# Kernel tuning notes

Hardware: AMD Instinct MI355X
Metric: run time of the kernel (lower is better)

Reference implementation:

```python
import jax, jax.numpy as jnp
import numpy as np

ALPHA = 0.01
EPSB = ALPHA / (1.0 - 2.0 * ALPHA)  # boundary_eps
BIG = 1e9  # stands in for +inf; all real boundary distances are << box diameter


def setup_inputs() -> dict:
    key = jax.random.key(0)
    ks = jax.random.split(key, 8)
    B, D, K = 32768, 16, 1024
    return {
        "x": jax.random.normal(ks[0], (B, D), jnp.float32),
        "logp": jnp.zeros((B, 1), jnp.float32),
        "an1_w": 0.1 * jax.random.normal(ks[1], (D,), jnp.float32),
        "an1_b": 0.1 * jax.random.normal(ks[2], (D,), jnp.float32),
        "an2_w": 0.1 * jax.random.normal(ks[3], (D,), jnp.float32),
        "an2_b": 0.1 * jax.random.normal(ks[4], (D,), jnp.float32),
        "shift_coeff": jax.random.normal(ks[5], (D,), jnp.float32),
        "anchor_raw": jax.random.normal(ks[6], (1, K, D), jnp.float32),  # vorproj._anchor_pts
        "box_min": -4.0 * jnp.ones((D,), jnp.float32),
        "box_max": 4.0 * jnp.ones((D,), jnp.float32),
        "mixture_logits": jnp.zeros((K,), jnp.float32),
    }


def reference(x, logp, an1_w, an1_b, an2_w, an2_b, shift_coeff,
              anchor_raw, box_min, box_max, mixture_logits):
    B, D = x.shape
    # --- actnorm1: y = (x + b) * exp(w); logdet = sum(w) ---
    x = (x + an1_b) * jnp.exp(an1_w)
    logp = logp - jnp.sum(an1_w)
    # --- logit_transform.inverse: y = (sigmoid(x) - alpha) / (1 - 2*alpha) ---
    ld = jnp.sum(jax.nn.log_sigmoid(x) + jax.nn.log_sigmoid(-x), axis=1, keepdims=True) \
         - D * jnp.log(1.0 - 2.0 * ALPHA)
    x = (jax.nn.sigmoid(x) - ALPHA) / (1.0 - 2.0 * ALPHA)
    logp = logp - ld
    # --- (-eps, 1+eps) -> (0, 1) ---
    span = 1.0 + 2.0 * EPSB
    x = (x + EPSB) / span
    logp = logp + D * jnp.log(span)
    # --- scale into box constraints ---
    scale = box_max - box_min  # (D,)
    x = x * scale + box_min
    logp = logp - jnp.sum(jnp.log(scale))
    # --- anchor points: R -> (-1,1) -> (0,1) -> box ---
    a = anchor_raw[0]                       # (K, D)
    a = a / (1.0 + jnp.abs(a))
    a = (a + 1.0) * 0.5 * scale + box_min   # (K, D)
    K = a.shape[0]
    # --- find_nearest: argmin_k ||x - a_k||^2 (drop const ||x||^2) ---
    a_sq = jnp.sum(a * a, axis=1)                    # (K,)
    d2 = a_sq[None, :] - 2.0 * (x @ a.T)             # (B, K)
    k = jnp.argmin(d2, axis=1)                       # (B,)
    mask = jax.nn.one_hot(k, K, dtype=bool).reshape(B, 1, K)
    x_k = a[k]                                       # (B, D) gathered anchor
    # --- shift toward anchor: x + c*(x_k - x); logdet = sum log(1-c) ---
    c = jax.nn.sigmoid(shift_coeff) * 0.98 + 0.01
    x = x + c * (x_k - x)
    logp = logp - jnp.sum(jnp.log1p(-c))
    # --- map_outside_cell: radial map of Voronoi cell (within box) onto R^D ---
    dx = x - x_k
    r = jnp.sqrt(jnp.sum(dx * dx, axis=1))           # (B,)
    u = dx / jnp.maximum(r, 1e-12)[:, None]          # (B, D) unit direction
    # half-plane boundary distance t_j = (||a_j - a_k||^2 / 2) / (u . (a_j - a_k))
    proj = u @ a.T - jnp.sum(u * x_k, axis=1, keepdims=True)              # (B, K)
    halfdist = 0.5 * (a_sq[None, :] + a_sq[k][:, None] - 2.0 * (x_k @ a.T))  # (B, K)
    self_mask = jnp.arange(K)[None, :] == k[:, None]
    valid = jnp.logical_and(jnp.logical_not(self_mask), proj > 1e-12)
    t_half = jnp.where(valid, halfdist / jnp.where(valid, proj, 1.0), BIG)
    # box-face distances along u
    up = u > 1e-12
    un = u < -1e-12
    t_box = jnp.where(up, (box_max[None, :] - x_k) / jnp.where(up, u, 1.0),
            jnp.where(un, (box_min[None, :] - x_k) / jnp.where(un, u, 1.0), BIG))
    t = jnp.minimum(jnp.min(t_half, axis=1), jnp.min(t_box, axis=1))      # (B,)
    ratio = r / t                                     # in [0, 0.99] after shift
    s = 1.0 / (1.0 - ratio)
    x = x_k + dx * s[:, None]
    # logdet = (D+1) * log(t / (t - r)) = -(D+1) * log1p(-ratio)
    logp = logp + (D + 1.0) * jnp.log1p(-ratio)[:, None]
    # --- subtract cell center ---
    x = x - x_k
    # --- actnorm2 ---
    x = (x + an2_b) * jnp.exp(an2_w)
    logp = logp - jnp.sum(an2_w)
    # --- mixture component log-prob ---
    logprobs = jax.nn.log_softmax(mixture_logits)
    logp = logp - logprobs[k][:, None]
    return x, logp, mask
```

## Files before the change

### kernel.cpp

```cpp
#include <hip/hip_runtime.h>
#include <math.h>

#define DD 16
#define KK 1024

typedef float f2 __attribute__((ext_vector_type(2)));

#define WS_A    0
#define WS_ASQ  16384
#define WS_OMC  17408
#define WS_B2   17424
#define WS_E2   17440
#define WS_MN   17456
#define WS_MX   17472
#define WS_SCL  17488
#define WS_DIM  17504
#define WS_E1   17520
#define WS_BASE 17536
#define WS_TOTD 17537
#define WS_NEED_BYTES (WS_TOTD * 8)

__device__ __forceinline__ double xformD(double rv, double mn, double scl) {
  double t = rv / (1.0 + fabs(rv));
  return (t + 1.0) * 0.5 * scl + mn;
}
__device__ __forceinline__ float xformF(float v, float mn, float mx) {
  return (v / (1.f + fabsf(v)) + 1.f) * 0.5f * (mx - mn) + mn;
}

__global__ __launch_bounds__(256) void vor_pre(
    const float* __restrict__ an1_w, const float* __restrict__ an2_w,
    const float* __restrict__ an2_b, const float* __restrict__ shift_c,
    const float* __restrict__ anchor_raw,
    const float* __restrict__ box_min, const float* __restrict__ box_max,
    const float* __restrict__ mlogits, double* __restrict__ ws)
{
  __shared__ double redD[16];
  const int tid = threadIdx.x;
  const int blk = blockIdx.x;

  if (blk == 0 && tid < DD) {
    double w1 = (double)an1_w[tid], w2 = (double)an2_w[tid];
    double sgc = 1.0 / (1.0 + exp(-(double)shift_c[tid]));
    double c = sgc * 0.98 + 0.01;
    double mn = (double)box_min[tid], mx = (double)box_max[tid];
    ws[WS_OMC + tid] = 1.0 - c;
    ws[WS_B2  + tid] = (double)an2_b[tid];
    ws[WS_E2  + tid] = exp(w2);
    ws[WS_MN  + tid] = mn;
    ws[WS_MX  + tid] = mx;
    ws[WS_SCL + tid] = mx - mn;
    ws[WS_E1  + tid] = exp(w1);
    ws[WS_DIM + tid] = -w1 - log(mx - mn) - log1p(-c) - w2;
  }
  const int j0 = blk * 64;
  for (int e = tid; e < 64 * DD; e += 256) {
    int j = j0 + (e >> 4), d = e & 15;
    double mn = (double)box_min[d];
    double scl = (double)box_max[d] - mn;
    ws[WS_A + (size_t)j * DD + d] = xformD((double)anchor_raw[j * DD + d], mn, scl);
  }
  __syncthreads();
  for (int j = j0 + tid; j < j0 + 64; j += 256) {
    double s = 0.0;
    #pragma unroll
    for (int d = 0; d < DD; ++d) { double a = ws[WS_A + (size_t)j * DD + d]; s = fma(a, a, s); }
    ws[WS_ASQ + j] = s;
  }
  if (blk != 0) return;
  float lm = -3.4e38f;
  for (int i = tid; i < KK; i += 256) lm = fmaxf(lm, mlogits[i]);
  #pragma unroll
  for (int o = 32; o > 0; o >>= 1) lm = fmaxf(lm, __shfl_xor(lm, o));
  if ((tid & 63) == 0) redD[tid >> 6] = (double)lm;
  __syncthreads();
  float gmax = (float)fmax(fmax(redD[0], redD[1]), fmax(redD[2], redD[3]));
  double lsum = 0.0;
  for (int i = tid; i < KK; i += 256) lsum += exp((double)mlogits[i] - (double)gmax);
  #pragma unroll
  for (int o = 32; o > 0; o >>= 1) lsum += __shfl_xor(lsum, o);
  if ((tid & 63) == 0) redD[4 + (tid >> 6)] = lsum;
  __syncthreads();
  if (tid == 0) {
    double lse = (double)gmax + log(redD[4] + redD[5] + redD[6] + redD[7]);
    double b = (double)DD * (log(0.98) + log(1.0 + 2.0 * (0.01 / 0.98)));
    #pragma unroll
    for (int d = 0; d < DD; ++d) b += ws[WS_DIM + d];
    ws[WS_BASE] = b + lse;
  }
}

#define NT2 1024
#define RPB2 128
#define SL2 8
#define JSL2 (KK / SL2)

__global__ __launch_bounds__(NT2, 4) void vor6(
    const float* __restrict__ x_in, const float* __restrict__ logp_in,
    const float* __restrict__ an1_b,
    const float* __restrict__ mlogits, const double* __restrict__ ws,
    float* __restrict__ out, int Brows)
{
  __shared__ __align__(16) float sAp[KK][DD];
  __shared__ float  sAsqH[KK];
  __shared__ double sX4D[DD][RPB2];
  __shared__ float  sLT[DD][RPB2];
  __shared__ double sD2[16][64];
  __shared__ int    sJJ[16][64];
  __shared__ float  sRat[16][64];
  __shared__ float  sOmcF[DD], sB2F[DD], sE2F[DD], sMnF[DD], sMxF[DD];

  const int tid  = threadIdx.x;
  const int w    = tid >> 6;
  const int lane = tid & 63;
  const int rg   = w >> 3;
  const int sl   = w & 7;
  const int rrow = rg * 64 + lane;
  const int row  = blockIdx.x * RPB2 + rrow;
  const size_t coreEnd = (size_t)Brows * (DD + 1);

  if (tid < DD) {
    sOmcF[tid] = (float)ws[WS_OMC + tid];
    sB2F[tid]  = (float)ws[WS_B2 + tid];
    sE2F[tid]  = (float)ws[WS_E2 + tid];
    sMnF[tid]  = (float)ws[WS_MN + tid];
    sMxF[tid]  = (float)ws[WS_MX + tid];
  }
  for (int e = tid; e < KK * DD; e += NT2) {
    int j = e >> 4, d = e & 15;
    float v = (float)ws[WS_A + (size_t)j * DD + d];
    int pos = (d < 8) ? (2 * d) : (2 * (d - 8) + 1);
    sAp[j][pos] = v;
  }
  {
    const double A = 0.01, EPSB = 0.01 / 0.98;
    const double SPAN = 1.0 + 2.0 * EPSB;
    const float* xb = x_in + (size_t)blockIdx.x * RPB2 * DD;
    for (int e = tid; e < RPB2 * DD; e += NT2) {
      int rr = e >> 4, d = e & 15;
      double y1 = ((double)xb[e] + (double)an1_b[d]) * ws[WS_E1 + d];
      double sg = 1.0 / (1.0 + exp(-y1));
      double x2 = (sg - A) / (1.0 - 2.0 * A);
      double x3 = (x2 + EPSB) / SPAN;
      double x4 = x3 * ws[WS_SCL + d] + ws[WS_MN + d];
      sX4D[d][rr] = x4;
      double ay = fabs(y1);
      sLT[d][rr] = (float)(ay + 2.0 * log1p(exp(-ay)));
    }
  }
  {
    float4* mz = (float4*)(out + coreEnd + (size_t)blockIdx.x * RPB2 * KK);
    #pragma unroll 4
    for (int i = tid; i < RPB2 * KK / 4; i += NT2)
      mz[i] = make_float4(0.f, 0.f, 0.f, 0.f);
  }
  __syncthreads();

  for (int j = tid; j < KK; j += NT2) {
    float a[DD];
    #pragma unroll
    for (int i = 0; i < 8; ++i) { a[i] = sAp[j][2 * i]; a[i + 8] = sAp[j][2 * i + 1]; }
    float acc = 0.f;
    #pragma unroll
    for (int d = 0; d < DD; ++d) acc = fmaf(a[d], a[d], acc);
    sAsqH[j] = 0.5f * acc;
  }

  float x4f[DD];
  #pragma unroll
  for (int d = 0; d < DD; ++d) x4f[d] = (float)sX4D[d][rrow];
  f2 x2p[8];
  #pragma unroll
  for (int i = 0; i < 8; ++i) x2p[i] = (f2){x4f[i], x4f[i + 8]};
  __syncthreads();

  const int jlo = sl * JSL2, jhi = jlo + JSL2;
  float m1 = -3.4e38f, m2v = -3.4e38f;
  int j1 = jlo, j2v = jlo;
  #pragma unroll 4
  for (int j = jlo; j < jhi; ++j) {
    const float4* ar = (const float4*)&sAp[j][0];
    float4 A0 = ar[0], A1 = ar[1], A2 = ar[2], A3 = ar[3];
    f2 acc = (f2){-sAsqH[j], 0.f};
    acc = __builtin_elementwise_fma(x2p[0], (f2){A0.x, A0.y}, acc);
    acc = __builtin_elementwise_fma(x2p[1], (f2){A0.z, A0.w}, acc);
    acc = __builtin_elementwise_fma(x2p[2], (f2){A1.x, A1.y}, acc);
    acc = __builtin_elementwise_fma(x2p[3], (f2){A1.z, A1.w}, acc);
    acc = __builtin_elementwise_fma(x2p[4], (f2){A2.x, A2.y}, acc);
    acc = __builtin_elementwise_fma(x2p[5], (f2){A2.z, A2.w}, acc);
    acc = __builtin_elementwise_fma(x2p[6], (f2){A3.x, A3.y}, acc);
    acc = __builtin_elementwise_fma(x2p[7], (f2){A3.z, A3.w}, acc);
    float m = acc.x + acc.y;
    bool gt1 = m > m1;
    bool gt2 = m > m2v;
    m2v = gt1 ? m1 : (gt2 ? m : m2v);
    j2v = gt1 ? j1 : (gt2 ? j : j2v);
    m1  = gt1 ? m : m1;
    j1  = gt1 ? j : j1;
  }

  {
    double bestD = 1e300; int bk = 0x7fffffff;
    #pragma unroll
    for (int t = 0; t < 2; ++t) {
      int j = t ? j2v : j1;
      const double* aj = ws + WS_A + (size_t)j * DD;
      double dot = 0.0;
      #pragma unroll
      for (int d = 0; d < DD; ++d) dot = fma(sX4D[d][rrow], aj[d], dot);
      double d2 = ws[WS_ASQ + j] - 2.0 * dot;
      if (d2 < bestD || (d2 == bestD && j < bk)) { bestD = d2; bk = j; }
    }
    sD2[w][lane] = bestD;
    sJJ[w][lane] = bk;
  }
  __syncthreads();

  int k = 0x7fffffff;
  {
    double kb = 1e300;
    #pragma unroll
    for (int ss = 0; ss < SL2; ++ss) {
      double d = sD2[rg * 8 + ss][lane];
      int    j = sJJ[rg * 8 + ss][lane];
      if (d < kb || (d == kb && j < k)) { kb = d; k = j; }
    }
  }

  float akf[DD];
  {
    const float4* akp = (const float4*)&sAp[k][0];
    float4 K0 = akp[0], K1 = akp[1], K2 = akp[2], K3 = akp[3];
    akf[0] = K0.x; akf[8]  = K0.y; akf[1] = K0.z; akf[9]  = K0.w;
    akf[2] = K1.x; akf[10] = K1.y; akf[3] = K1.z; akf[11] = K1.w;
    akf[4] = K2.x; akf[12] = K2.y; akf[5] = K2.z; akf[13] = K2.w;
    akf[6] = K3.x; akf[14] = K3.y; akf[7] = K3.z; akf[15] = K3.w;
  }
  float dxf[DD];
  float r2f = 0.f, dxak = 0.f;
  #pragma unroll
  for (int d = 0; d < DD; ++d) {
    float dx = sOmcF[d] * (x4f[d] - akf[d]);
    dxf[d] = dx;
    r2f  = fmaf(dx, dx, r2f);
    dxak = fmaf(dx, akf[d], dxak);
  }
  const float rf   = sqrtf(r2f);
  const float rrf  = fmaxf(rf, 1e-12f);
  const float scal = rf / rrf;
  const float epsr = 1e-12f * rf;
  const float asqhk = sAsqH[k];

  f2 dx2[8], nak2[8];
  #pragma unroll
  for (int i = 0; i < 8; ++i) {
    dx2[i]  = (f2){dxf[i], dxf[i + 8]};
    nak2[i] = (f2){-akf[i], -akf[i + 8]};
  }

  float q1 = 0.f, h1 = 1.f;
  #pragma unroll 2
  for (int j = jlo; j < jhi; ++j) {
    const float4* ar = (const float4*)&sAp[j][0];
    float4 A0 = ar[0], A1 = ar[1], A2 = ar[2], A3 = ar[3];
    f2 p0 = (f2){A0.x, A0.y}, p1 = (f2){A0.z, A0.w};
    f2 p2 = (f2){A1.x, A1.y}, p3 = (f2){A1.z, A1.w};
    f2 p4 = (f2){A2.x, A2.y}, p5 = (f2){A2.z, A2.w};
    f2 p6 = (f2){A3.x, A3.y}, p7 = (f2){A3.z, A3.w};
    f2 q2 = (f2){-dxak, 0.f};
    f2 h2 = (f2){asqhk + sAsqH[j], 0.f};
    q2 = __builtin_elementwise_fma(dx2[0], p0, q2); h2 = __builtin_elementwise_fma(nak2[0], p0, h2);
    q2 = __builtin_elementwise_fma(dx2[1], p1, q2); h2 = __builtin_elementwise_fma(nak2[1], p1, h2);
    q2 = __builtin_elementwise_fma(dx2[2], p2, q2); h2 = __builtin_elementwise_fma(nak2[2], p2, h2);
    q2 = __builtin_elementwise_fma(dx2[3], p3, q2); h2 = __builtin_elementwise_fma(nak2[3], p3, h2);
    q2 = __builtin_elementwise_fma(dx2[4], p4, q2); h2 = __builtin_elementwise_fma(nak2[4], p4, h2);
    q2 = __builtin_elementwise_fma(dx2[5], p5, q2); h2 = __builtin_elementwise_fma(nak2[5], p5, h2);
    q2 = __builtin_elementwise_fma(dx2[6], p6, q2); h2 = __builtin_elementwise_fma(nak2[6], p6, h2);
    q2 = __builtin_elementwise_fma(dx2[7], p7, q2); h2 = __builtin_elementwise_fma(nak2[7], p7, h2);
    float q = q2.x + q2.y, h = h2.x + h2.y;
    bool upd = (j != k) & (q > epsr) & (q * h1 > q1 * h);
    q1 = upd ? q : q1;
    h1 = upd ? h : h1;
  }
  sRat[w][lane] = scal * (q1 / h1);
  __syncthreads();

  if (sl == 0) {
    float ratio = rf * 1e-9f;
    #pragma unroll
    for (int ss = 0; ss < SL2; ++ss) ratio = fmaxf(ratio, sRat[rg * 8 + ss][lane]);
    #pragma unroll
    for (int d = 0; d < DD; ++d) {
      float uf = dxf[d] / rrf;
      if (uf > 1e-12f)        ratio = fmaxf(ratio, rf * uf / (sMxF[d] - akf[d]));
      else if (uf < -1e-12f)  ratio = fmaxf(ratio, rf * uf / (sMnF[d] - akf[d]));
    }
    float sS = 1.0f / (1.0f - ratio);
    float xo[DD];
    float lsig = 0.f;
    #pragma unroll
    for (int d = 0; d < DD; ++d) {
      xo[d] = (dxf[d] * sS + sB2F[d]) * sE2F[d];
      lsig += sLT[d][rrow];
    }
    float4* xp = (float4*)(out + (size_t)row * DD);
    xp[0] = make_float4(xo[0], xo[1], xo[2], xo[3]);
    xp[1] = make_float4(xo[4], xo[5], xo[6], xo[7]);
    xp[2] = make_float4(xo[8], xo[9], xo[10], xo[11]);
    xp[3] = make_float4(xo[12], xo[13], xo[14], xo[15]);
    double lp = (double)logp_in[row] + ws[WS_BASE] + (double)lsig
              + 17.0 * log1p(-(double)ratio)
              - (double)mlogits[k];
    out[(size_t)Brows * DD + row] = (float)lp;
    out[coreEnd + (size_t)row * KK + k] = 1.0f;
  }
}

#define NT 256
#define RPB 64
#define SLC4 4
#define JSL4 (KK / SLC4)

__global__ __launch_bounds__(NT, 2) void vor_green(
    const float* __restrict__ x_in, const float* __restrict__ logp_in,
    const float* __restrict__ an1_w, const float* __restrict__ an1_b,
    const float* __restrict__ an2_w, const float* __restrict__ an2_b,
    const float* __restrict__ shift_c, const float* __restrict__ anchor_raw,
    const float* __restrict__ box_min, const float* __restrict__ box_max,
    const float* __restrict__ mlogits,
    float* __restrict__ out, int Brows)
{
  __shared__ __align__(16) float sA[KK][DD];
  __shared__ float  sAsqH[KK];
  __shared__ float  sX4T[DD][RPB];
  __shared__ int    sPj1[SLC4][RPB], sPj2[SLC4][RPB];
  __shared__ int    sRI1[SLC4][RPB], sRI2[SLC4][RPB];
  __shared__ double sPartD[8];
  __shared__ double sE1D[DD], sB1D[DD], sOmcD[DD], sB2D[DD], sE2D[DD];
  __shared__ double sMnD[DD], sMxD[DD], sSclD[DD], sDimD[DD];
  __shared__ double sBaseD;
  __shared__ int    sKidx[RPB];

  const int tid  = threadIdx.x;
  const int sl   = tid >> 6;
  const int lane = tid & 63;
  const int row  = blockIdx.x * RPB + lane;
  const size_t coreEnd = (size_t)Brows * (DD + 1);

  for (int e = tid; e < KK * DD / 4; e += NT) {
    float4 raw = ((const float4*)anchor_raw)[e];
    float4 bmn = ((const float4*)box_min)[e & 3];
    float4 bmx = ((const float4*)box_max)[e & 3];
    float4 o;
    o.x = xformF(raw.x, bmn.x, bmx.x);
    o.y = xformF(raw.y, bmn.y, bmx.y);
    o.z = xformF(raw.z, bmn.z, bmx.z);
    o.w = xformF(raw.w, bmn.w, bmx.w);
    ((float4*)sA)[e] = o;
  }
  if (tid < DD) {
    double w1 = (double)an1_w[tid];
    sE1D[tid] = exp(w1);
    sB1D[tid] = (double)an1_b[tid];
    double sgc = 1.0 / (1.0 + exp(-(double)shift_c[tid]));
    double c = sgc * 0.98 + 0.01;
    sOmcD[tid] = 1.0 - c;
    double mn = (double)box_min[tid], mx = (double)box_max[tid];
    sMnD[tid] = mn; sMxD[tid] = mx; sSclD[tid] = mx - mn;
    double w2 = (double)an2_w[tid];
    sE2D[tid] = exp(w2);
    sB2D[tid] = (double)an2_b[tid];
    sDimD[tid] = -w1 - log(mx - mn) - log1p(-c) - w2;
  }
  __syncthreads();

  for (int j = tid; j < KK; j += NT) {
    float acc = 0.f;
    #pragma unroll
    for (int d = 0; d < DD; ++d) { float a = sA[j][d]; acc = fmaf(a, a, acc); }
    sAsqH[j] = 0.5f * acc;
  }

  float lm = -3.4e38f;
  for (int i = tid; i < KK; i += NT) lm = fmaxf(lm, mlogits[i]);
  #pragma unroll
  for (int o = 32; o > 0; o >>= 1) lm = fmaxf(lm, __shfl_xor(lm, o));
  if (lane == 0) sPartD[sl] = (double)lm;
  __syncthreads();
  float gmax = (float)fmax(fmax(sPartD[0], sPartD[1]), fmax(sPartD[2], sPartD[3]));
  double lsum = 0.0;
  for (int i = tid; i < KK; i += NT) lsum += exp((double)mlogits[i] - (double)gmax);
  #pragma unroll
  for (int o = 32; o > 0; o >>= 1) lsum += __shfl_xor(lsum, o);
  if (lane == 0) sPartD[4 + sl] = lsum;
  __syncthreads();
  if (tid == 0) {
    double lse = (double)gmax + log(sPartD[4] + sPartD[5] + sPartD[6] + sPartD[7]);
    double b = (double)DD * (log(0.98) + log(1.0 + 2.0 * (0.01 / 0.98)));
    #pragma unroll
    for (int d = 0; d < DD; ++d) b += sDimD[d];
    sBaseD = b + lse;
  }

  double x4d[DD];
  double lsigD = 0.0;
  if (sl == 0) {
    const double A = 0.01, EPSB = 0.01 / 0.98;
    const double SPAN = 1.0 + 2.0 * EPSB;
    const float* xr = x_in + (size_t)row * DD;
    #pragma unroll
    for (int d = 0; d < DD; ++d) {
      double y1 = ((double)xr[d] + sB1D[d]) * sE1D[d];
      double sg = 1.0 / (1.0 + exp(-y1));
      double x2 = (sg - A) / (1.0 - 2.0 * A);
      double x3 = (x2 + EPSB) / SPAN;
      double x4 = x3 * sSclD[d] + sMnD[d];
      x4d[d] = x4;
      sX4T[d][lane] = (float)x4;
      double ay = fabs(y1);
      lsigD += ay + 2.0 * log1p(exp(-ay));
    }
  }
  {
    float4* mz = (float4*)(out + coreEnd + (size_t)blockIdx.x * RPB * KK);
    #pragma unroll 4
    for (int i = tid; i < RPB * KK / 4; i += NT)
      mz[i] = make_float4(0.f, 0.f, 0.f, 0.f);
  }
  __syncthreads();

  float x4f[DD];
  #pragma unroll
  for (int d = 0; d < DD; ++d) x4f[d] = sX4T[d][lane];

  float m1 = -3.4e38f, m2v = -3.4e38f;
  int j1 = 0x7fffffff, j2v = 0x7fffffff;
  const int jlo = sl * JSL4, jhi = jlo + JSL4;
  #pragma unroll 2
  for (int j = jlo; j < jhi; ++j) {
    float acc = -sAsqH[j];
    const float4* ar = (const float4*)&sA[j][0];
    #pragma unroll
    for (int dq = 0; dq < 4; ++dq) {
      float4 a4 = ar[dq];
      acc = fmaf(x4f[4 * dq + 0], a4.x, acc);
      acc = fmaf(x4f[4 * dq + 1], a4.y, acc);
      acc = fmaf(x4f[4 * dq + 2], a4.z, acc);
      acc = fmaf(x4f[4 * dq + 3], a4.w, acc);
    }
    bool gt1 = acc > m1;
    bool gt2 = acc > m2v;
    m2v = gt1 ? m1 : (gt2 ? acc : m2v);
    j2v = gt1 ? j1 : (gt2 ? j : j2v);
    m1  = gt1 ? acc : m1;
    j1  = gt1 ? j : j1;
  }
  sPj1[sl][lane] = j1;
  sPj2[sl][lane] = j2v;
  __syncthreads();

  if (sl == 0) {
    double best = 1e300; int bk = 0x7fffffff;
    #pragma unroll
    for (int ss = 0; ss < SLC4; ++ss) {
      #pragma unroll
      for (int t = 0; t < 2; ++t) {
        int j = t ? sPj2[ss][lane] : sPj1[ss][lane];
        double asq = 0.0, dot = 0.0;
        #pragma unroll
        for (int d = 0; d < DD; ++d) {
          double a = xformD((double)anchor_raw[j * DD + d], sMnD[d], sSclD[d]);
          asq = fma(a, a, asq);
          dot = fma(x4d[d], a, dot);
        }
        double d2 = asq - 2.0 * dot;
        if (d2 < best || (d2 == best && j < bk)) { best = d2; bk = j; }
      }
    }
    sKidx[lane] = bk;
  }
  __syncthreads();

  const int k = sKidx[lane];

  float akf[DD], dxf[DD];
  float r2f = 0.f, dxak = 0.f;
  #pragma unroll
  for (int d = 0; d < DD; ++d) {
    float a = sA[k][d];
    akf[d] = a;
    float dx = (float)sOmcD[d] * (x4f[d] - a);
    dxf[d] = dx;
    r2f  = fmaf(dx, dx, r2f);
    dxak = fmaf(dx, a, dxak);
  }
  const float epsr = 1e-12f * sqrtf(r2f);
  const float asqhk = sAsqH[k];

  float q1 = 0.f, h1 = 1.f, q2 = 0.f, h2 = 1.f;
  int i1 = -1, i2 = -1;
  #pragma unroll 2
  for (int j = jlo; j < jhi; ++j) {
    float q = -dxak;
    float h = asqhk + sAsqH[j];
    const float4* ar = (const float4*)&sA[j][0];
    #pragma unroll
    for (int dq = 0; dq < 4; ++dq) {
      float4 a4 = ar[dq];
      q = fmaf(dxf[4 * dq + 0], a4.x, q);
      q = fmaf(dxf[4 * dq + 1], a4.y, q);
      q = fmaf(dxf[4 * dq + 2], a4.z, q);
      q = fmaf(dxf[4 * dq + 3], a4.w, q);
      h = fmaf(-akf[4 * dq + 0], a4.x, h);
      h = fmaf(-akf[4 * dq + 1], a4.y, h);
      h = fmaf(-akf[4 * dq + 2], a4.z, h);
      h = fmaf(-akf[4 * dq + 3], a4.w, h);
    }
    bool valid = (j != k) & (q > epsr);
    bool b1 = valid && (q * h1 > q1 * h);
    bool b2 = valid && (q * h2 > q2 * h);
    float nq2 = b1 ? q1 : (b2 ? q : q2);
    float nh2 = b1 ? h1 : (b2 ? h : h2);
    int   ni2 = b1 ? i1 : (b2 ? j : i2);
    q1 = b1 ? q : q1; h1 = b1 ? h : h1; i1 = b1 ? j : i1;
    q2 = nq2; h2 = nh2; i2 = ni2;
  }
  sRI1[sl][lane] = i1;
  sRI2[sl][lane] = i2;
  __syncthreads();

  if (sl == 0) {
    double akD[DD], dxD[DD];
    double r2 = 0.0;
    #pragma unroll
    for (int d = 0; d < DD; ++d) {
      double a = xformD((double)anchor_raw[k * DD + d], sMnD[d], sSclD[d]);
      akD[d] = a;
      double dx = sOmcD[d] * (x4d[d] - a);
      dxD[d] = dx;
      r2 = fma(dx, dx, r2);
    }
    double rD = sqrt(r2);
    double rr = fmax(rD, 1e-12);
    double ratio = rD / 1e9;

    #pragma unroll
    for (int ss = 0; ss < SLC4; ++ss) {
      #pragma unroll
      for (int t = 0; t < 2; ++t) {
        int j = t ? sRI2[ss][lane] : sRI1[ss][lane];
        if (j < 0 || j == k) continue;
        double q = 0.0, h = 0.0;
        #pragma unroll
        for (int d = 0; d < DD; ++d) {
          double aj = xformD((double)anchor_raw[j * DD + d], sMnD[d], sSclD[d]);
          double g = aj - akD[d];
          q = fma(dxD[d], g, q);
          h = fma(g, g, h);
        }
        double proj = q / rr;
        if (proj > 1e-12) {
          double cand = rD * proj / (0.5 * h);
          ratio = fmax(ratio, cand);
        }
      }
    }
    #pragma unroll
    for (int d = 0; d < DD; ++d) {
      double u = dxD[d] / rr;
      if (u > 1e-12)        ratio = fmax(ratio, rD * u / (sMxD[d] - akD[d]));
      else if (u < -1e-12)  ratio = fmax(ratio, rD * u / (sMnD[d] - akD[d]));
    }

    double sS = 1.0 / (1.0 - ratio);
    float* xo = out + (size_t)row * DD;
    #pragma unroll
    for (int d = 0; d < DD; ++d) {
      double x7 = dxD[d] * sS;
      double x8 = (x7 + sB2D[d]) * sE2D[d];
      xo[d] = (float)x8;
    }
    double lp = (double)logp_in[row] + sBaseD + lsigD
              + 17.0 * log1p(-ratio)
              - (double)mlogits[k];
    out[(size_t)Brows * DD + row] = (float)lp;
    out[coreEnd + (size_t)row * KK + k] = 1.0f;
  }
}

extern "C" void kernel_launch(void* const* d_in, const int* in_sizes, int n_in,
                              void* d_out, int out_size, void* d_ws, size_t ws_size,
                              hipStream_t stream) {
  (void)n_in; (void)out_size;
  const float* x_in   = (const float*)d_in[0];
  const float* logp   = (const float*)d_in[1];
  const float* an1w   = (const float*)d_in[2];
  const float* an1b   = (const float*)d_in[3];
  const float* an2w   = (const float*)d_in[4];
  const float* an2b   = (const float*)d_in[5];
  const float* shiftc = (const float*)d_in[6];
  const float* anchor = (const float*)d_in[7];
  const float* bmin   = (const float*)d_in[8];
  const float* bmax   = (const float*)d_in[9];
  const float* mlog   = (const float*)d_in[10];
  const int B = in_sizes[0] / DD;

  if (ws_size >= (size_t)WS_NEED_BYTES && d_ws != nullptr && (B % RPB2) == 0) {
    double* ws = (double*)d_ws;
    hipLaunchKernelGGL(vor_pre, dim3(16), dim3(256), 0, stream,
                       an1w, an2w, an2b, shiftc, anchor, bmin, bmax, mlog, ws);
    hipLaunchKernelGGL(vor6, dim3(B / RPB2), dim3(NT2), 0, stream,
                       x_in, logp, an1b, mlog,
                       (const double*)ws, (float*)d_out, B);
  } else {
    hipLaunchKernelGGL(vor_green, dim3(B / RPB), dim3(NT), 0, stream,
                       x_in, logp, an1w, an1b, an2w, an2b, shiftc, anchor,
                       bmin, bmax, mlog, (float*)d_out, B);
  }
}
```

Baseline: 97.00 us.

## Process two rows per thread across sixteen anchor slices for register reuse

The work split in the Voronoi kernel changes from one row per thread across 8 anchor slices to two rows per thread across 16 slices of 64 anchors. Each anchor vector loaded from shared memory is now reused for two rows in both the nearest-anchor search and the half-plane scan, which halves LDS reads per FMA. The cost is roughly double the register use per thread under launch bounds of 1024 threads, which may cause spills. The final reduction and output writes are done by wave 0 alone over 16 slices for two rows each, so that serial tail gets longer.

```diff
diff --git a/kernel.cpp b/kernel.cpp
--- a/kernel.cpp
+++ b/kernel.cpp
@@ -92,10 +92,10 @@
 
 #define NT2 1024
 #define RPB2 128
-#define SL2 8
-#define JSL2 (KK / SL2)
-
-__global__ __launch_bounds__(NT2, 4) void vor6(
+#define NSL 16
+#define JSL 64
+
+__global__ __launch_bounds__(NT2, 4) void vor7(
     const float* __restrict__ x_in, const float* __restrict__ logp_in,
     const float* __restrict__ an1_b,
     const float* __restrict__ mlogits, const double* __restrict__ ws,
@@ -105,18 +105,17 @@
   __shared__ float  sAsqH[KK];
   __shared__ double sX4D[DD][RPB2];
   __shared__ float  sLT[DD][RPB2];
-  __shared__ double sD2[16][64];
-  __shared__ int    sJJ[16][64];
-  __shared__ float  sRat[16][64];
+  __shared__ double sD2[NSL][RPB2];
+  __shared__ int    sJJ[NSL][RPB2];
+  __shared__ float  sRat[NSL][RPB2];
   __shared__ float  sOmcF[DD], sB2F[DD], sE2F[DD], sMnF[DD], sMxF[DD];
 
   const int tid  = threadIdx.x;
   const int w    = tid >> 6;
   const int lane = tid & 63;
-  const int rg   = w >> 3;
-  const int sl   = w & 7;
-  const int rrow = rg * 64 + lane;
-  const int row  = blockIdx.x * RPB2 + rrow;
+  const int r0   = lane, r1 = lane + 64;
+  const int row0 = blockIdx.x * RPB2 + r0;
+  const int row1 = blockIdx.x * RPB2 + r1;
   const size_t coreEnd = (size_t)Brows * (DD + 1);
 
   if (tid < DD) {
@@ -166,99 +165,20 @@
     sAsqH[j] = 0.5f * acc;
   }
 
-  float x4f[DD];
-  #pragma unroll
-  for (int d = 0; d < DD; ++d) x4f[d] = (float)sX4D[d][rrow];
-  f2 x2p[8];
-  #pragma unroll
-  for (int i = 0; i < 8; ++i) x2p[i] = (f2){x4f[i], x4f[i + 8]};
-  __syncthreads();
-
-  const int jlo = sl * JSL2, jhi = jlo + JSL2;
-  float m1 = -3.4e38f, m2v = -3.4e38f;
-  int j1 = jlo, j2v = jlo;
-  #pragma unroll 4
-  for (int j = jlo; j < jhi; ++j) {
-    const float4* ar = (const float4*)&sAp[j][0];
-    float4 A0 = ar[0], A1 = ar[1], A2 = ar[2], A3 = ar[3];
-    f2 acc = (f2){-sAsqH[j], 0.f};
-    acc = __builtin_elementwise_fma(x2p[0], (f2){A0.x, A0.y}, acc);
-    acc = __builtin_elementwise_fma(x2p[1], (f2){A0.z, A0.w}, acc);
-    acc = __builtin_elementwise_fma(x2p[2], (f2){A1.x, A1.y}, acc);
-    acc = __builtin_elementwise_fma(x2p[3], (f2){A1.z, A1.w}, acc);
-    acc = __builtin_elementwise_fma(x2p[4], (f2){A2.x, A2.y}, acc);
-    acc = __builtin_elementwise_fma(x2p[5], (f2){A2.z, A2.w}, acc);
-    acc = __builtin_elementwise_fma(x2p[6], (f2){A3.x, A3.y}, acc);
-    acc = __builtin_elementwise_fma(x2p[7], (f2){A3.z, A3.w}, acc);
-    float m = acc.x + acc.y;
-    bool gt1 = m > m1;
-    bool gt2 = m > m2v;
-    m2v = gt1 ? m1 : (gt2 ? m : m2v);
-    j2v = gt1 ? j1 : (gt2 ? j : j2v);
-    m1  = gt1 ? m : m1;
-    j1  = gt1 ? j : j1;
-  }
-
-  {
-    double bestD = 1e300; int bk = 0x7fffffff;
-    #pragma unroll
-    for (int t = 0; t < 2; ++t) {
-      int j = t ? j2v : j1;
-      const double* aj = ws + WS_A + (size_t)j * DD;
-      double dot = 0.0;
-      #pragma unroll
-      for (int d = 0; d < DD; ++d) dot = fma(sX4D[d][rrow], aj[d], dot);
-      double d2 = ws[WS_ASQ + j] - 2.0 * dot;
-      if (d2 < bestD || (d2 == bestD && j < bk)) { bestD = d2; bk = j; }
-    }
-    sD2[w][lane] = bestD;
-    sJJ[w][lane] = bk;
-  }
-  __syncthreads();
-
-  int k = 0x7fffffff;
-  {
-    double kb = 1e300;
-    #pragma unroll
-    for (int ss = 0; ss < SL2; ++ss) {
-      double d = sD2[rg * 8 + ss][lane];
-      int    j = sJJ[rg * 8 + ss][lane];
-      if (d < kb || (d == kb && j < k)) { kb = d; k = j; }
-    }
-  }
-
-  float akf[DD];
-  {
-    const float4* akp = (const float4*)&sAp[k][0];
-    float4 K0 = akp[0], K1 = akp[1], K2 = akp[2], K3 = akp[3];
-    akf[0] = K0.x; akf[8]  = K0.y; akf[1] = K0.z; akf[9]  = K0.w;
-    akf[2] = K1.x; akf[10] = K1.y; akf[3] = K1.z; akf[11] = K1.w;
-    akf[4] = K2.x; akf[12] = K2.y; akf[5] = K2.z; akf[13] = K2.w;
-    akf[6] = K3.x; akf[14] = K3.y; akf[7] = K3.z; akf[15] = K3.w;
-  }
-  float dxf[DD];
-  float r2f = 0.f, dxak = 0.f;
-  #pragma unroll
-  for (int d = 0; d < DD; ++d) {
-    float dx = sOmcF[d] * (x4f[d] - akf[d]);
-    dxf[d] = dx;
-    r2f  = fmaf(dx, dx, r2f);
-    dxak = fmaf(dx, akf[d], dxak);
-  }
-  const float rf   = sqrtf(r2f);
-  const float rrf  = fmaxf(rf, 1e-12f);
-  const float scal = rf / rrf;
-  const float epsr = 1e-12f * rf;
-  const float asqhk = sAsqH[k];
-
-  f2 dx2[8], nak2[8];
+  float x4f0[DD], x4f1[DD];
+  #pragma unroll
+  for (int d = 0; d < DD; ++d) { x4f0[d] = (float)sX4D[d][r0]; x4f1[d] = (float)sX4D[d][r1]; }
+  f2 xp0[8], xp1[8];
   #pragma unroll
   for (int i = 0; i < 8; ++i) {
-    dx2[i]  = (f2){dxf[i], dxf[i + 8]};
-    nak2[i] = (f2){-akf[i], -akf[i + 8]};
-  }
-
-  float q1 = 0.f, h1 = 1.f;
+    xp0[i] = (f2){x4f0[i], x4f0[i + 8]};
+    xp1[i] = (f2){x4f1[i], x4f1[i + 8]};
+  }
+  __syncthreads();
+
+  const int jlo = w * JSL, jhi = jlo + JSL;
+  float m1_0 = -3.4e38f, m2_0 = -3.4e38f; int j1_0 = jlo, j2_0 = jlo;
+  float m1_1 = -3.4e38f, m2_1 = -3.4e38f; int j1_1 = jlo, j2_1 = jlo;
   #pragma unroll 2
   for (int j = jlo; j < jhi; ++j) {
     const float4* ar = (const float4*)&sAp[j][0];
@@ -267,52 +187,217 @@
     f2 p2 = (f2){A1.x, A1.y}, p3 = (f2){A1.z, A1.w};
     f2 p4 = (f2){A2.x, A2.y}, p5 = (f2){A2.z, A2.w};
     f2 p6 = (f2){A3.x, A3.y}, p7 = (f2){A3.z, A3.w};
-    f2 q2 = (f2){-dxak, 0.f};
-    f2 h2 = (f2){asqhk + sAsqH[j], 0.f};
-    q2 = __builtin_elementwise_fma(dx2[0], p0, q2); h2 = __builtin_elementwise_fma(nak2[0], p0, h2);
-    q2 = __builtin_elementwise_fma(dx2[1], p1, q2); h2 = __builtin_elementwise_fma(nak2[1], p1, h2);
-    q2 = __builtin_elementwise_fma(dx2[2], p2, q2); h2 = __builtin_elementwise_fma(nak2[2], p2, h2);
-    q2 = __builtin_elementwise_fma(dx2[3], p3, q2); h2 = __builtin_elementwise_fma(nak2[3], p3, h2);
-    q2 = __builtin_elementwise_fma(dx2[4], p4, q2); h2 = __builtin_elementwise_fma(nak2[4], p4, h2);
-    q2 = __builtin_elementwise_fma(dx2[5], p5, q2); h2 = __builtin_elementwise_fma(nak2[5], p5, h2);
-    q2 = __builtin_elementwise_fma(dx2[6], p6, q2); h2 = __builtin_elementwise_fma(nak2[6], p6, h2);
-    q2 = __builtin_elementwise_fma(dx2[7], p7, q2); h2 = __builtin_elementwise_fma(nak2[7], p7, h2);
-    float q = q2.x + q2.y, h = h2.x + h2.y;
-    bool upd = (j != k) & (q > epsr) & (q * h1 > q1 * h);
-    q1 = upd ? q : q1;
-    h1 = upd ? h : h1;
-  }
-  sRat[w][lane] = scal * (q1 / h1);
-  __syncthreads();
-
-  if (sl == 0) {
-    float ratio = rf * 1e-9f;
-    #pragma unroll
-    for (int ss = 0; ss < SL2; ++ss) ratio = fmaxf(ratio, sRat[rg * 8 + ss][lane]);
-    #pragma unroll
-    for (int d = 0; d < DD; ++d) {
-      float uf = dxf[d] / rrf;
-      if (uf > 1e-12f)        ratio = fmaxf(ratio, rf * uf / (sMxF[d] - akf[d]));
-      else if (uf < -1e-12f)  ratio = fmaxf(ratio, rf * uf / (sMnF[d] - akf[d]));
-    }
-    float sS = 1.0f / (1.0f - ratio);
-    float xo[DD];
-    float lsig = 0.f;
-    #pragma unroll
-    for (int d = 0; d < DD; ++d) {
-      xo[d] = (dxf[d] * sS + sB2F[d]) * sE2F[d];
-      lsig += sLT[d][rrow];
-    }
-    float4* xp = (float4*)(out + (size_t)row * DD);
-    xp[0] = make_float4(xo[0], xo[1], xo[2], xo[3]);
-    xp[1] = make_float4(xo[4], xo[5], xo[6], xo[7]);
-    xp[2] = make_float4(xo[8], xo[9], xo[10], xo[11]);
-    xp[3] = make_float4(xo[12], xo[13], xo[14], xo[15]);
-    double lp = (double)logp_in[row] + ws[WS_BASE] + (double)lsig
-              + 17.0 * log1p(-(double)ratio)
-              - (double)mlogits[k];
-    out[(size_t)Brows * DD + row] = (float)lp;
-    out[coreEnd + (size_t)row * KK + k] = 1.0f;
+    float nq = -sAsqH[j];
+    f2 a0 = (f2){nq, 0.f}, a1 = (f2){nq, 0.f};
+    a0 = __builtin_elementwise_fma(xp0[0], p0, a0); a1 = __builtin_elementwise_fma(xp1[0], p0, a1);
+    a0 = __builtin_elementwise_fma(xp0[1], p1, a0); a1 = __builtin_elementwise_fma(xp1[1], p1, a1);
+    a0 = __builtin_elementwise_fma(xp0[2], p2, a0); a1 = __builtin_elementwise_fma(xp1[2], p2, a1);
+    a0 = __builtin_elementwise_fma(xp0[3], p3, a0); a1 = __builtin_elementwise_fma(xp1[3], p3, a1);
+    a0 = __builtin_elementwise_fma(xp0[4], p4, a0); a1 = __builtin_elementwise_fma(xp1[4], p4, a1);
+    a0 = __builtin_elementwise_fma(xp0[5], p5, a0); a1 = __builtin_elementwise_fma(xp1[5], p5, a1);
+    a0 = __builtin_elementwise_fma(xp0[6], p6, a0); a1 = __builtin_elementwise_fma(xp1[6], p6, a1);
+    a0 = __builtin_elementwise_fma(xp0[7], p7, a0); a1 = __builtin_elementwise_fma(xp1[7], p7, a1);
+    float s0 = a0.x + a0.y, s1 = a1.x + a1.y;
+    bool g1 = s0 > m1_0, g2 = s0 > m2_0;
+    m2_0 = g1 ? m1_0 : (g2 ? s0 : m2_0);
+    j2_0 = g1 ? j1_0 : (g2 ? j : j2_0);
+    m1_0 = g1 ? s0 : m1_0;
+    j1_0 = g1 ? j : j1_0;
+    bool h1b = s1 > m1_1, h2b = s1 > m2_1;
+    m2_1 = h1b ? m1_1 : (h2b ? s1 : m2_1);
+    j2_1 = h1b ? j1_1 : (h2b ? j : j2_1);
+    m1_1 = h1b ? s1 : m1_1;
+    j1_1 = h1b ? j : j1_1;
+  }
+
+  {
+    double bD = 1e300; int bk = 0x7fffffff;
+    #pragma unroll
+    for (int t = 0; t < 2; ++t) {
+      int j = t ? j2_0 : j1_0;
+      const double* aj = ws + WS_A + (size_t)j * DD;
+      double dot = 0.0;
+      #pragma unroll
+      for (int d = 0; d < DD; ++d) dot = fma(sX4D[d][r0], aj[d], dot);
+      double d2 = ws[WS_ASQ + j] - 2.0 * dot;
+      if (d2 < bD || (d2 == bD && j < bk)) { bD = d2; bk = j; }
+    }
+    sD2[w][r0] = bD; sJJ[w][r0] = bk;
+  }
+  {
+    double bD = 1e300; int bk = 0x7fffffff;
+    #pragma unroll
+    for (int t = 0; t < 2; ++t) {
+      int j = t ? j2_1 : j1_1;
+      const double* aj = ws + WS_A + (size_t)j * DD;
+      double dot = 0.0;
+      #pragma unroll
+      for (int d = 0; d < DD; ++d) dot = fma(sX4D[d][r1], aj[d], dot);
+      double d2 = ws[WS_ASQ + j] - 2.0 * dot;
+      if (d2 < bD || (d2 == bD && j < bk)) { bD = d2; bk = j; }
+    }
+    sD2[w][r1] = bD; sJJ[w][r1] = bk;
+  }
+  __syncthreads();
+
+  int k0 = 0x7fffffff, k1 = 0x7fffffff;
+  {
+    double kb0 = 1e300, kb1 = 1e300;
+    #pragma unroll
+    for (int ss = 0; ss < NSL; ++ss) {
+      double d0 = sD2[ss][r0]; int jj0 = sJJ[ss][r0];
+      if (d0 < kb0 || (d0 == kb0 && jj0 < k0)) { kb0 = d0; k0 = jj0; }
+      double d1 = sD2[ss][r1]; int jj1 = sJJ[ss][r1];
+      if (d1 < kb1 || (d1 == kb1 && jj1 < k1)) { kb1 = d1; k1 = jj1; }
+    }
+  }
+
+  float akf0[DD], akf1[DD];
+  {
+    const float4* ap = (const float4*)&sAp[k0][0];
+    float4 K0 = ap[0], K1 = ap[1], K2 = ap[2], K3 = ap[3];
+    akf0[0]=K0.x; akf0[8]=K0.y; akf0[1]=K0.z; akf0[9]=K0.w;
+    akf0[2]=K1.x; akf0[10]=K1.y; akf0[3]=K1.z; akf0[11]=K1.w;
+    akf0[4]=K2.x; akf0[12]=K2.y; akf0[5]=K2.z; akf0[13]=K2.w;
+    akf0[6]=K3.x; akf0[14]=K3.y; akf0[7]=K3.z; akf0[15]=K3.w;
+  }
+  {
+    const float4* ap = (const float4*)&sAp[k1][0];
+    float4 K0 = ap[0], K1 = ap[1], K2 = ap[2], K3 = ap[3];
+    akf1[0]=K0.x; akf1[8]=K0.y; akf1[1]=K0.z; akf1[9]=K0.w;
+    akf1[2]=K1.x; akf1[10]=K1.y; akf1[3]=K1.z; akf1[11]=K1.w;
+    akf1[4]=K2.x; akf1[12]=K2.y; akf1[5]=K2.z; akf1[13]=K2.w;
+    akf1[6]=K3.x; akf1[14]=K3.y; akf1[7]=K3.z; akf1[15]=K3.w;
+  }
+  float dxf0[DD], dxf1[DD];
+  float r2_0 = 0.f, dk_0 = 0.f, r2_1 = 0.f, dk_1 = 0.f;
+  #pragma unroll
+  for (int d = 0; d < DD; ++d) {
+    float dx0 = sOmcF[d] * (x4f0[d] - akf0[d]);
+    dxf0[d] = dx0;
+    r2_0 = fmaf(dx0, dx0, r2_0);
+    dk_0 = fmaf(dx0, akf0[d], dk_0);
+    float dx1 = sOmcF[d] * (x4f1[d] - akf1[d]);
+    dxf1[d] = dx1;
+    r2_1 = fmaf(dx1, dx1, r2_1);
+    dk_1 = fmaf(dx1, akf1[d], dk_1);
+  }
+  const float rf0 = sqrtf(r2_0), rr0 = fmaxf(rf0, 1e-12f), sc0 = rf0 / rr0, ep0 = 1e-12f * rf0;
+  const float rf1 = sqrtf(r2_1), rr1 = fmaxf(rf1, 1e-12f), sc1 = rf1 / rr1, ep1 = 1e-12f * rf1;
+  const float ah0 = sAsqH[k0], ah1 = sAsqH[k1];
+
+  f2 dxp0[8], dxp1[8], nk0[8], nk1[8];
+  #pragma unroll
+  for (int i = 0; i < 8; ++i) {
+    dxp0[i] = (f2){dxf0[i], dxf0[i + 8]};
+    dxp1[i] = (f2){dxf1[i], dxf1[i + 8]};
+    nk0[i]  = (f2){-akf0[i], -akf0[i + 8]};
+    nk1[i]  = (f2){-akf1[i], -akf1[i + 8]};
+  }
+
+  float q1_0 = 0.f, h1_0 = 1.f, q1_1 = 0.f, h1_1 = 1.f;
+  for (int j = jlo; j < jhi; ++j) {
+    const float4* ar = (const float4*)&sAp[j][0];
+    float4 A0 = ar[0], A1 = ar[1], A2 = ar[2], A3 = ar[3];
+    f2 p0 = (f2){A0.x, A0.y}, p1 = (f2){A0.z, A0.w};
+    f2 p2 = (f2){A1.x, A1.y}, p3 = (f2){A1.z, A1.w};
+    f2 p4 = (f2){A2.x, A2.y}, p5 = (f2){A2.z, A2.w};
+    f2 p6 = (f2){A3.x, A3.y}, p7 = (f2){A3.z, A3.w};
+    float aj = sAsqH[j];
+    f2 q0 = (f2){-dk_0, 0.f}, h0 = (f2){ah0 + aj, 0.f};
+    f2 q1v = (f2){-dk_1, 0.f}, h1v = (f2){ah1 + aj, 0.f};
+    q0 = __builtin_elementwise_fma(dxp0[0], p0, q0); h0 = __builtin_elementwise_fma(nk0[0], p0, h0);
+    q1v = __builtin_elementwise_fma(dxp1[0], p0, q1v); h1v = __builtin_elementwise_fma(nk1[0], p0, h1v);
+    q0 = __builtin_elementwise_fma(dxp0[1], p1, q0); h0 = __builtin_elementwise_fma(nk0[1], p1, h0);
+    q1v = __builtin_elementwise_fma(dxp1[1], p1, q1v); h1v = __builtin_elementwise_fma(nk1[1], p1, h1v);
+    q0 = __builtin_elementwise_fma(dxp0[2], p2, q0); h0 = __builtin_elementwise_fma(nk0[2], p2, h0);
+    q1v = __builtin_elementwise_fma(dxp1[2], p2, q1v); h1v = __builtin_elementwise_fma(nk1[2], p2, h1v);
+    q0 = __builtin_elementwise_fma(dxp0[3], p3, q0); h0 = __builtin_elementwise_fma(nk0[3], p3, h0);
+    q1v = __builtin_elementwise_fma(dxp1[3], p3, q1v); h1v = __builtin_elementwise_fma(nk1[3], p3, h1v);
+    q0 = __builtin_elementwise_fma(dxp0[4], p4, q0); h0 = __builtin_elementwise_fma(nk0[4], p4, h0);
+    q1v = __builtin_elementwise_fma(dxp1[4], p4, q1v); h1v = __builtin_elementwise_fma(nk1[4], p4, h1v);
+    q0 = __builtin_elementwise_fma(dxp0[5], p5, q0); h0 = __builtin_elementwise_fma(nk0[5], p5, h0);
+    q1v = __builtin_elementwise_fma(dxp1[5], p5, q1v); h1v = __builtin_elementwise_fma(nk1[5], p5, h1v);
+    q0 = __builtin_elementwise_fma(dxp0[6], p6, q0); h0 = __builtin_elementwise_fma(nk0[6], p6, h0);
+    q1v = __builtin_elementwise_fma(dxp1[6], p6, q1v); h1v = __builtin_elementwise_fma(nk1[6], p6, h1v);
+    q0 = __builtin_elementwise_fma(dxp0[7], p7, q0); h0 = __builtin_elementwise_fma(nk0[7], p7, h0);
+    q1v = __builtin_elementwise_fma(dxp1[7], p7, q1v); h1v = __builtin_elementwise_fma(nk1[7], p7, h1v);
+    {
+      float q = q0.x + q0.y, h = h0.x + h0.y;
+      bool upd = (j != k0) & (q > ep0) & (q * h1_0 > q1_0 * h);
+      q1_0 = upd ? q : q1_0;
+      h1_0 = upd ? h : h1_0;
+    }
+    {
+      float q = q1v.x + q1v.y, h = h1v.x + h1v.y;
+      bool upd = (j != k1) & (q > ep1) & (q * h1_1 > q1_1 * h);
+      q1_1 = upd ? q : q1_1;
+      h1_1 = upd ? h : h1_1;
+    }
+  }
+  sRat[w][r0] = sc0 * (q1_0 / h1_0);
+  sRat[w][r1] = sc1 * (q1_1 / h1_1);
+  __syncthreads();
+
+  if (w == 0) {
+    {
+      float ratio = rf0 * 1e-9f;
+      #pragma unroll
+      for (int ss = 0; ss < NSL; ++ss) ratio = fmaxf(ratio, sRat[ss][r0]);
+      #pragma unroll
+      for (int d = 0; d < DD; ++d) {
+        float uf = dxf0[d] / rr0;
+        if (uf > 1e-12f)        ratio = fmaxf(ratio, rf0 * uf / (sMxF[d] - akf0[d]));
+        else if (uf < -1e-12f)  ratio = fmaxf(ratio, rf0 * uf / (sMnF[d] - akf0[d]));
+      }
+      float sS = 1.0f / (1.0f - ratio);
+      float xo[DD];
+      float lsig = 0.f;
+      #pragma unroll
+      for (int d = 0; d < DD; ++d) {
+        xo[d] = (dxf0[d] * sS + sB2F[d]) * sE2F[d];
+        lsig += sLT[d][r0];
+      }
+      float4* xp = (float4*)(out + (size_t)row0 * DD);
+      xp[0] = make_float4(xo[0], xo[1], xo[2], xo[3]);
+      xp[1] = make_float4(xo[4], xo[5], xo[6], xo[7]);
+      xp[2] = make_float4(xo[8], xo[9], xo[10], xo[11]);
+      xp[3] = make_float4(xo[12], xo[13], xo[14], xo[15]);
+      double lp = (double)logp_in[row0] + ws[WS_BASE] + (double)lsig
+                + 17.0 * log1p(-(double)ratio)
+                - (double)mlogits[k0];
+      out[(size_t)Brows * DD + row0] = (float)lp;
+      out[coreEnd + (size_t)row0 * KK + k0] = 1.0f;
+    }
+    {
+      float ratio = rf1 * 1e-9f;
+      #pragma unroll
+      for (int ss = 0; ss < NSL; ++ss) ratio = fmaxf(ratio, sRat[ss][r1]);
+      #pragma unroll
+      for (int d = 0; d < DD; ++d) {
+        float uf = dxf1[d] / rr1;
+        if (uf > 1e-12f)        ratio = fmaxf(ratio, rf1 * uf / (sMxF[d] - akf1[d]));
+        else if (uf < -1e-12f)  ratio = fmaxf(ratio, rf1 * uf / (sMnF[d] - akf1[d]));
+      }
+      float sS = 1.0f / (1.0f - ratio);
+      float xo[DD];
+      float lsig = 0.f;
+      #pragma unroll
+      for (int d = 0; d < DD; ++d) {
+        xo[d] = (dxf1[d] * sS + sB2F[d]) * sE2F[d];
+        lsig += sLT[d][r1];
+      }
+      float4* xp = (float4*)(out + (size_t)row1 * DD);
+      xp[0] = make_float4(xo[0], xo[1], xo[2], xo[3]);
+      xp[1] = make_float4(xo[4], xo[5], xo[6], xo[7]);
+      xp[2] = make_float4(xo[8], xo[9], xo[10], xo[11]);
+      xp[3] = make_float4(xo[12], xo[13], xo[14], xo[15]);
+      double lp = (double)logp_in[row1] + ws[WS_BASE] + (double)lsig
+                + 17.0 * log1p(-(double)ratio)
+                - (double)mlogits[k1];
+      out[(size_t)Brows * DD + row1] = (float)lp;
+      out[coreEnd + (size_t)row1 * KK + k1] = 1.0f;
+    }
   }
 }
 
@@ -609,7 +694,7 @@
     double* ws = (double*)d_ws;
     hipLaunchKernelGGL(vor_pre, dim3(16), dim3(256), 0, stream,
                        an1w, an2w, an2b, shiftc, anchor, bmin, bmax, mlog, ws);
-    hipLaunchKernelGGL(vor6, dim3(B / RPB2), dim3(NT2), 0, stream,
+    hipLaunchKernelGGL(vor7, dim3(B / RPB2), dim3(NT2), 0, stream,
                        x_in, logp, an1b, mlog,
                        (const double*)ws, (float*)d_out, B);
   } else {
```

Result: slower. 104.4 us (+7.6%).

## Register-block nearest-anchor search over two rows per thread with 16 anchor slices

Applied to the files above, without the earlier changes.

The argmin phase now has each thread handle two rows (lane and lane+64) against a 64-anchor slice. Previously each thread handled one row against a 128-anchor slice. Each anchor loaded from LDS is reused for two rows, which halves shared-memory reads per FMA. The cost is more registers for the second row's state, two double-precision refinements per thread, and a 16-way instead of 8-way merge through larger shared buffers.

```diff
diff --git a/kernel.cpp b/kernel.cpp
--- a/kernel.cpp
+++ b/kernel.cpp
@@ -94,8 +94,10 @@
 #define RPB2 128
 #define SL2 8
 #define JSL2 (KK / SL2)
-
-__global__ __launch_bounds__(NT2, 4) void vor6(
+#define NS1 16
+#define JS1 (KK / NS1)
+
+__global__ __launch_bounds__(NT2, 4) void vor8(
     const float* __restrict__ x_in, const float* __restrict__ logp_in,
     const float* __restrict__ an1_b,
     const float* __restrict__ mlogits, const double* __restrict__ ws,
@@ -105,8 +107,8 @@
   __shared__ float  sAsqH[KK];
   __shared__ double sX4D[DD][RPB2];
   __shared__ float  sLT[DD][RPB2];
-  __shared__ double sD2[16][64];
-  __shared__ int    sJJ[16][64];
+  __shared__ double sD2[NS1][RPB2];
+  __shared__ int    sJJ[NS1][RPB2];
   __shared__ float  sRat[16][64];
   __shared__ float  sOmcF[DD], sB2F[DD], sE2F[DD], sMnF[DD], sMxF[DD];
 
@@ -116,6 +118,7 @@
   const int rg   = w >> 3;
   const int sl   = w & 7;
   const int rrow = rg * 64 + lane;
+  const int r0   = lane, r1 = lane + 64;
   const int row  = blockIdx.x * RPB2 + rrow;
   const size_t coreEnd = (size_t)Brows * (DD + 1);
 
@@ -166,53 +169,76 @@
     sAsqH[j] = 0.5f * acc;
   }
 
-  float x4f[DD];
-  #pragma unroll
-  for (int d = 0; d < DD; ++d) x4f[d] = (float)sX4D[d][rrow];
-  f2 x2p[8];
-  #pragma unroll
-  for (int i = 0; i < 8; ++i) x2p[i] = (f2){x4f[i], x4f[i + 8]};
-  __syncthreads();
-
-  const int jlo = sl * JSL2, jhi = jlo + JSL2;
-  float m1 = -3.4e38f, m2v = -3.4e38f;
-  int j1 = jlo, j2v = jlo;
-  #pragma unroll 4
-  for (int j = jlo; j < jhi; ++j) {
-    const float4* ar = (const float4*)&sAp[j][0];
-    float4 A0 = ar[0], A1 = ar[1], A2 = ar[2], A3 = ar[3];
-    f2 acc = (f2){-sAsqH[j], 0.f};
-    acc = __builtin_elementwise_fma(x2p[0], (f2){A0.x, A0.y}, acc);
-    acc = __builtin_elementwise_fma(x2p[1], (f2){A0.z, A0.w}, acc);
-    acc = __builtin_elementwise_fma(x2p[2], (f2){A1.x, A1.y}, acc);
-    acc = __builtin_elementwise_fma(x2p[3], (f2){A1.z, A1.w}, acc);
-    acc = __builtin_elementwise_fma(x2p[4], (f2){A2.x, A2.y}, acc);
-    acc = __builtin_elementwise_fma(x2p[5], (f2){A2.z, A2.w}, acc);
-    acc = __builtin_elementwise_fma(x2p[6], (f2){A3.x, A3.y}, acc);
-    acc = __builtin_elementwise_fma(x2p[7], (f2){A3.z, A3.w}, acc);
-    float m = acc.x + acc.y;
-    bool gt1 = m > m1;
-    bool gt2 = m > m2v;
-    m2v = gt1 ? m1 : (gt2 ? m : m2v);
-    j2v = gt1 ? j1 : (gt2 ? j : j2v);
-    m1  = gt1 ? m : m1;
-    j1  = gt1 ? j : j1;
-  }
+  f2 xp0[8], xp1[8];
+  #pragma unroll
+  for (int i = 0; i < 8; ++i) {
+    xp0[i] = (f2){(float)sX4D[i][r0], (float)sX4D[i + 8][r0]};
+    xp1[i] = (f2){(float)sX4D[i][r1], (float)sX4D[i + 8][r1]};
+  }
+  __syncthreads();
 
   {
-    double bestD = 1e300; int bk = 0x7fffffff;
-    #pragma unroll
-    for (int t = 0; t < 2; ++t) {
-      int j = t ? j2v : j1;
-      const double* aj = ws + WS_A + (size_t)j * DD;
-      double dot = 0.0;
+    const int jlo = w * JS1, jhi = jlo + JS1;
+    float m1_0 = -3.4e38f, m2_0 = -3.4e38f; int j1_0 = jlo, j2_0 = jlo;
+    float m1_1 = -3.4e38f, m2_1 = -3.4e38f; int j1_1 = jlo, j2_1 = jlo;
+    #pragma unroll 2
+    for (int j = jlo; j < jhi; ++j) {
+      const float4* ar = (const float4*)&sAp[j][0];
+      float4 A0 = ar[0], A1 = ar[1], A2 = ar[2], A3 = ar[3];
+      f2 p0 = (f2){A0.x, A0.y}, p1 = (f2){A0.z, A0.w};
+      f2 p2 = (f2){A1.x, A1.y}, p3 = (f2){A1.z, A1.w};
+      f2 p4 = (f2){A2.x, A2.y}, p5 = (f2){A2.z, A2.w};
+      f2 p6 = (f2){A3.x, A3.y}, p7 = (f2){A3.z, A3.w};
+      float nq = -sAsqH[j];
+      f2 a0 = (f2){nq, 0.f}, a1 = (f2){nq, 0.f};
+      a0 = __builtin_elementwise_fma(xp0[0], p0, a0); a1 = __builtin_elementwise_fma(xp1[0], p0, a1);
+      a0 = __builtin_elementwise_fma(xp0[1], p1, a0); a1 = __builtin_elementwise_fma(xp1[1], p1, a1);
+      a0 = __builtin_elementwise_fma(xp0[2], p2, a0); a1 = __builtin_elementwise_fma(xp1[2], p2, a1);
+      a0 = __builtin_elementwise_fma(xp0[3], p3, a0); a1 = __builtin_elementwise_fma(xp1[3], p3, a1);
+      a0 = __builtin_elementwise_fma(xp0[4], p4, a0); a1 = __builtin_elementwise_fma(xp1[4], p4, a1);
+      a0 = __builtin_elementwise_fma(xp0[5], p5, a0); a1 = __builtin_elementwise_fma(xp1[5], p5, a1);
+      a0 = __builtin_elementwise_fma(xp0[6], p6, a0); a1 = __builtin_elementwise_fma(xp1[6], p6, a1);
+      a0 = __builtin_elementwise_fma(xp0[7], p7, a0); a1 = __builtin_elementwise_fma(xp1[7], p7, a1);
+      float s0 = a0.x + a0.y, s1 = a1.x + a1.y;
+      bool g1 = s0 > m1_0, g2 = s0 > m2_0;
+      m2_0 = g1 ? m1_0 : (g2 ? s0 : m2_0);
+      j2_0 = g1 ? j1_0 : (g2 ? j : j2_0);
+      m1_0 = g1 ? s0 : m1_0;
+      j1_0 = g1 ? j : j1_0;
+      bool h1b = s1 > m1_1, h2b = s1 > m2_1;
+      m2_1 = h1b ? m1_1 : (h2b ? s1 : m2_1);
+      j2_1 = h1b ? j1_1 : (h2b ? j : j2_1);
+      m1_1 = h1b ? s1 : m1_1;
+      j1_1 = h1b ? j : j1_1;
+    }
+    {
+      double bD = 1e300; int bk = 0x7fffffff;
       #pragma unroll
-      for (int d = 0; d < DD; ++d) dot = fma(sX4D[d][rrow], aj[d], dot);
-      double d2 = ws[WS_ASQ + j] - 2.0 * dot;
-      if (d2 < bestD || (d2 == bestD && j < bk)) { bestD = d2; bk = j; }
-    }
-    sD2[w][lane] = bestD;
-    sJJ[w][lane] = bk;
+      for (int t = 0; t < 2; ++t) {
+        int j = t ? j2_0 : j1_0;
+        const double* aj = ws + WS_A + (size_t)j * DD;
+        double dot = 0.0;
+        #pragma unroll
+        for (int d = 0; d < DD; ++d) dot = fma(sX4D[d][r0], aj[d], dot);
+        double d2 = ws[WS_ASQ + j] - 2.0 * dot;
+        if (d2 < bD || (d2 == bD && j < bk)) { bD = d2; bk = j; }
+      }
+      sD2[w][r0] = bD; sJJ[w][r0] = bk;
+    }
+    {
+      double bD = 1e300; int bk = 0x7fffffff;
+      #pragma unroll
+      for (int t = 0; t < 2; ++t) {
+        int j = t ? j2_1 : j1_1;
+        const double* aj = ws + WS_A + (size_t)j * DD;
+        double dot = 0.0;
+        #pragma unroll
+        for (int d = 0; d < DD; ++d) dot = fma(sX4D[d][r1], aj[d], dot);
+        double d2 = ws[WS_ASQ + j] - 2.0 * dot;
+        if (d2 < bD || (d2 == bD && j < bk)) { bD = d2; bk = j; }
+      }
+      sD2[w][r1] = bD; sJJ[w][r1] = bk;
+    }
   }
   __syncthreads();
 
@@ -220,13 +246,16 @@
   {
     double kb = 1e300;
     #pragma unroll
-    for (int ss = 0; ss < SL2; ++ss) {
-      double d = sD2[rg * 8 + ss][lane];
-      int    j = sJJ[rg * 8 + ss][lane];
+    for (int ss = 0; ss < NS1; ++ss) {
+      double d = sD2[ss][rrow];
+      int    j = sJJ[ss][rrow];
       if (d < kb || (d == kb && j < k)) { kb = d; k = j; }
     }
   }
 
+  float x4f[DD];
+  #pragma unroll
+  for (int d = 0; d < DD; ++d) x4f[d] = (float)sX4D[d][rrow];
   float akf[DD];
   {
     const float4* akp = (const float4*)&sAp[k][0];
@@ -259,8 +288,9 @@
   }
 
   float q1 = 0.f, h1 = 1.f;
+  const int jlo2 = sl * JSL2, jhi2 = jlo2 + JSL2;
   #pragma unroll 2
-  for (int j = jlo; j < jhi; ++j) {
+  for (int j = jlo2; j < jhi2; ++j) {
     const float4* ar = (const float4*)&sAp[j][0];
     float4 A0 = ar[0], A1 = ar[1], A2 = ar[2], A3 = ar[3];
     f2 p0 = (f2){A0.x, A0.y}, p1 = (f2){A0.z, A0.w};
@@ -609,7 +639,7 @@
     double* ws = (double*)d_ws;
     hipLaunchKernelGGL(vor_pre, dim3(16), dim3(256), 0, stream,
                        an1w, an2w, an2b, shiftc, anchor, bmin, bmax, mlog, ws);
-    hipLaunchKernelGGL(vor6, dim3(B / RPB2), dim3(NT2), 0, stream,
+    hipLaunchKernelGGL(vor8, dim3(B / RPB2), dim3(NT2), 0, stream,
                        x_in, logp, an1b, mlog,
                        (const double*)ws, (float*)d_out, B);
   } else {
```

New measurement: 97.85 us. No clear change (+0.9%).
